# Kernel tuning notes

Hardware: AMD Instinct MI355X
Metric: run time of the kernel (lower is better)

Reference implementation:

```python
import jax, jax.numpy as jnp
import numpy as np

D, HALF, HID, COND, NBLK = 784, 392, 512, 10, 20
CLAMP = 1.0
B = 4096


def _linear_params(key, fan_in, fan_out, n):
    kw, kb = jax.random.split(key)
    lim = 1.0 / np.sqrt(fan_in)
    W = jax.random.uniform(kw, (n, fan_in, fan_out), minval=-lim, maxval=lim, dtype=jnp.float32)
    b = jax.random.uniform(kb, (n, fan_out), minval=-lim, maxval=lim, dtype=jnp.float32)
    return W, b


def setup_inputs() -> dict:
    key = jax.random.key(0)
    ks = jax.random.split(key, 6)
    x = jax.random.normal(ks[0], (B, 1, 28, 28), dtype=jnp.float32)
    l = jax.random.randint(ks[1], (B,), 0, 10)
    # FrEIA PermuteRandom: fixed permutation from numpy seed k per block
    perms = jnp.asarray(np.stack([np.random.RandomState(k).permutation(D) for k in range(NBLK)]), dtype=jnp.int32)
    s1_W1, s1_b1 = _linear_params(ks[2], HALF + COND, HID, NBLK)
    s1_W2, s1_b2 = _linear_params(ks[3], HID, 2 * HALF, NBLK)
    s2_W1, s2_b1 = _linear_params(ks[4], HALF + COND, HID, NBLK)
    s2_W2, s2_b2 = _linear_params(ks[5], HID, 2 * HALF, NBLK)
    return dict(x=x, l=l, perms=perms,
                s1_W1=s1_W1, s1_b1=s1_b1, s1_W2=s1_W2, s1_b2=s1_b2,
                s2_W1=s2_W1, s2_b1=s2_b1, s2_W2=s2_W2, s2_b2=s2_b2)


def _log_e(s):
    # FrEIA GLOW clamping: clamp * 0.636 * atan(s / clamp)
    return CLAMP * 0.636 * jnp.arctan(s / CLAMP)


def reference(x, l, perms, s1_W1, s1_b1, s1_W2, s1_b2, s2_W1, s2_b1, s2_W2, s2_b2):
    v = x.reshape(x.shape[0], D)  # Flatten
    c = jax.nn.one_hot(l, COND, dtype=v.dtype)  # one_hot condition [B,10]
    jac0 = jnp.zeros(v.shape[0], dtype=v.dtype)

    def block(carry, p):
        v, jac = carry
        perm, W1a, b1a, W1b, b1b, W2a, b2a, W2b, b2b = p
        v = v[:, perm]  # PermuteRandom (log-det 0)
        x1, x2 = v[:, :HALF], v[:, HALF:]
        # GLOWCouplingBlock forward
        r2 = jax.nn.relu(jnp.concatenate([x2, c], 1) @ W2a + b2a) @ W2b + b2b
        s2, t2 = r2[:, :HALF], r2[:, HALF:]
        ls2 = _log_e(s2)
        y1 = jnp.exp(ls2) * x1 + t2
        r1 = jax.nn.relu(jnp.concatenate([y1, c], 1) @ W1a + b1a) @ W1b + b1b
        s1, t1 = r1[:, :HALF], r1[:, HALF:]
        ls1 = _log_e(s1)
        y2 = jnp.exp(ls1) * x2 + t1
        jac = jac + ls1.sum(1) + ls2.sum(1)
        return (jnp.concatenate([y1, y2], 1), jac), None

    (z, jac), _ = jax.lax.scan(
        block, (v, jac0),
        (perms, s1_W1, s1_b1, s1_W2, s1_b2, s2_W1, s2_b1, s2_W2, s2_b2))
    return z, jac
```

## Files before the change

### kernel.cpp

```cpp
#include <hip/hip_runtime.h>

#define BN 4096
#define DF 784
#define HALFF 392
#define HIDF 512
#define NBLK 20
#define KS1 448
#define KS2 512
#define BT 16
#define NW 8
#define THREADS 512

#define Y1o 28672
#define Y2o 35840
#define Ho  43008
#define SMH 51200

typedef _Float16 f16;
typedef _Float16 half4v __attribute__((ext_vector_type(4)));
typedef _Float16 half8v __attribute__((ext_vector_type(8)));
typedef float    fx4    __attribute__((ext_vector_type(4)));
typedef int      ix4    __attribute__((ext_vector_type(4)));

__device__ __forceinline__ int lad(int base, int b, int k, int pitch)
{
    return base + b * pitch + (k & ~63) + ((((k >> 3) & 7) ^ (b & 7)) << 3) + (k & 7);
}

__global__ void pack1_k(const float* __restrict__ W1, f16* __restrict__ dst)
{
    const int m = blockIdx.y;
    const int nt = blockIdx.x / 14, sl = blockIdx.x % 14;
    const int l = threadIdx.x;
    const int n = nt * 16 + (l & 15);
    const int kb = sl * 32 + (l >> 4) * 8;
    const float* src = W1 + (long)m * 402 * 512;
    half8v o;
    #pragma unroll
    for (int e = 0; e < 8; e++) {
        int k = kb + e;
        o[e] = (k < HALFF) ? (f16)src[(long)k * 512 + n] : (f16)0.f;
    }
    *(half8v*)&dst[(((long)(m * 32 + nt) * 14) + sl) * 512 + l * 8] = o;
}

__global__ void pack2_k(const float* __restrict__ W2, f16* __restrict__ dst)
{
    const int m = blockIdx.y;
    const int dt = blockIdx.x / 16, sl = blockIdx.x % 16;
    const int c = threadIdx.x >> 6, l = threadIdx.x & 63;
    int dr = dt * 16 + (l & 15);
    if (dr >= HALFF) dr = HALFF - 1;
    const int d = dr + c * HALFF;
    const int kb = sl * 32 + (l >> 4) * 8;
    const float* src = W2 + (long)m * 512 * 784;
    half8v o;
    #pragma unroll
    for (int e = 0; e < 8; e++)
        o[e] = (f16)src[(long)(kb + e) * 784 + d];
    *(half8v*)&dst[((((long)(m * 25 + dt) * 16) + sl) * 2 + c) * 512 + l * 8] = o;
}

__global__ void prep_c16_k(const float* __restrict__ W1, const float* __restrict__ b1,
                           f16* __restrict__ dst)
{
    const int m = blockIdx.x;
    for (int idx = threadIdx.x; idx < 10 * HIDF; idx += 256) {
        int cls = idx >> 9, n = idx & 511;
        dst[(long)m * 10 * HIDF + idx] =
            (f16)(W1[(long)m * 402 * 512 + (long)(HALFF + cls) * 512 + n] + b1[(long)m * HIDF + n]);
    }
}

__global__ void inv_k(const int* __restrict__ perms, int* __restrict__ invp)
{
    const int i = blockIdx.x;
    for (int d = threadIdx.x; d < DF; d += 256) {
        int src = perms[(long)i * DF + d];
        invp[(long)i * DF + src] = d;
    }
}

__device__ __forceinline__ void do_gemm1(f16* SM, const f16* __restrict__ Wpk,
                                         const f16* __restrict__ C16,
                                         int Ao, int clsr, int wid, int lane,
                                         int ln16, int koct)
{
    half8v afr[14];
    #pragma unroll
    for (int sl = 0; sl < 14; sl++)
        afr[sl] = *(const half8v*)&SM[lad(Ao, ln16, sl * 32 + koct * 8, KS1)];

    const f16* base = Wpk + (long)wid * 4 * 14 * 512 + lane * 8;
    half8v wf[2][14];
    #pragma unroll
    for (int sl = 0; sl < 14; sl++)
        wf[0][sl] = *(const half8v*)&base[sl * 512];

    #pragma unroll
    for (int j = 0; j < 4; j++) {
        if (j < 3) {
            const f16* bn = base + (j + 1) * 14 * 512;
            #pragma unroll
            for (int sl = 0; sl < 14; sl++)
                wf[(j + 1) & 1][sl] = *(const half8v*)&bn[sl * 512];
        }
        fx4 acc = {};
        #pragma unroll
        for (int sl = 0; sl < 14; sl++)
            acc = __builtin_amdgcn_mfma_f32_16x16x32_f16(wf[j & 1][sl], afr[sl], acc, 0, 0, 0);
        int nb = wid * 64 + j * 16 + koct * 4;
        half4v c = *(const half4v*)&C16[clsr * HIDF + nb];
        half4v o;
        #pragma unroll
        for (int r = 0; r < 4; r++)
            o[r] = (f16)fmaxf(acc[r] + (float)c[r], 0.f);
        *(half4v*)&SM[lad(Ho, ln16, nb, HIDF)] = o;
    }
}

__device__ __forceinline__ float couple_store(f16* SM, const float* __restrict__ b2,
        const int* __restrict__ invz, int B1o_, int B2o_, int doScat,
        int Xmo, int Yo, int dbase, int ln16, fx4 sac, fx4 tac)
{
    float jp = 0.f;
    if (dbase + 3 < HALFF) {
        fx4 bs = *(const fx4*)&b2[dbase];
        fx4 bt = *(const fx4*)&b2[dbase + HALFF];
        half4v xv = *(const half4v*)&SM[lad(Xmo, ln16, dbase, KS1)];
        half4v o;
        #pragma unroll
        for (int r = 0; r < 4; r++) {
            float s  = sac[r] + bs[r];
            float tt = tac[r] + bt[r];
            float ls = 0.636f * atanf(s);
            jp += ls;
            o[r] = (f16)(expf(ls) * (float)xv[r] + tt);
        }
        *(half4v*)&SM[lad(Yo, ln16, dbase, KS1)] = o;
        if (doScat) {
            ix4 iv = *(const ix4*)&invz[dbase];
            #pragma unroll
            for (int r = 0; r < 4; r++) {
                int dp = iv[r];
                int dbo = (dp < HALFF) ? B1o_ : B2o_;
                int dk  = (dp < HALFF) ? dp : dp - HALFF;
                SM[lad(dbo, ln16, dk, KS1)] = o[r];
            }
        }
    }
    return jp;
}

__device__ __forceinline__ float do_gemm2(f16* SM, const f16* __restrict__ Wpk,
        const float* __restrict__ b2, const int* __restrict__ invz,
        int B1o_, int B2o_, int doScat, int Xmo, int Yo,
        int wid, int lane, int ln16, int koct)
{
    float jp = 0.f;
    #pragma unroll
    for (int j = 0; j < 4; j++) {
        const int dp = (j < 3) ? (wid + j * 8) : 24;
        const bool act = (j < 3) || (wid == 0);
        if (act) {
            const f16* bp = Wpk + (long)dp * (16 * 2 * 512) + lane * 8;
            half8v ws[16], wt[16];
            #pragma unroll
            for (int sl = 0; sl < 16; sl++)
                ws[sl] = *(const half8v*)&bp[(sl * 2) * 512];
            #pragma unroll
            for (int sl = 0; sl < 16; sl++)
                wt[sl] = *(const half8v*)&bp[(sl * 2 + 1) * 512];
            fx4 sac = {}, tac = {};
            #pragma unroll
            for (int sl = 0; sl < 16; sl++) {
                half8v h = *(const half8v*)&SM[lad(Ho, ln16, sl * 32 + koct * 8, HIDF)];
                sac = __builtin_amdgcn_mfma_f32_16x16x32_f16(ws[sl], h, sac, 0, 0, 0);
                tac = __builtin_amdgcn_mfma_f32_16x16x32_f16(wt[sl], h, tac, 0, 0, 0);
            }
            jp += couple_store(SM, b2, invz, B1o_, B2o_, doScat, Xmo, Yo,
                               dp * 16 + koct * 4, ln16, sac, tac);
        }
    }
    return jp;
}

__global__ __launch_bounds__(THREADS, 2)
void mega_k(const float* __restrict__ x, const int* __restrict__ lvec,
            const int* __restrict__ invp,
            const f16* __restrict__ Wf1a, const f16* __restrict__ Wf1b,
            const f16* __restrict__ Wf2a, const f16* __restrict__ Wf2b,
            const f16* __restrict__ C16a, const f16* __restrict__ C16b,
            const float* __restrict__ b2a, const float* __restrict__ b2b,
            float* __restrict__ outp)
{
    __shared__ __align__(16) f16 SM[SMH];
    __shared__ float JR[NW][BT];
    const int tid  = threadIdx.x;
    const int wid  = tid >> 6, lane = tid & 63;
    const int ln16 = lane & 15, koct = lane >> 4;
    const int b0g  = blockIdx.x * BT;
    const int clsr = lvec[b0g + ln16];

    int A1 = 0, A2 = 7168, B1 = 14336, B2 = 21504;

    half8v hz = {};
    for (int idx = tid; idx < 3 * BT * 7; idx += THREADS) {
        int buf = idx / (BT * 7);
        int rem = idx - buf * (BT * 7);
        int b = rem / 7, g = rem - (rem / 7) * 7;
        int base = (buf == 0) ? A2 : (buf == 1) ? B2 : Y1o;
        *(half8v*)&SM[lad(base, b, HALFF + g * 8, KS1)] = hz;
    }
    for (int idx = tid; idx < BT * (DF / 4); idx += THREADS) {
        int b = idx / (DF / 4);
        int q = (idx - b * (DF / 4)) * 4;
        fx4 v = *(const fx4*)&x[(long)(b0g + b) * DF + q];
        ix4 iv = *(const ix4*)&invp[q];
        #pragma unroll
        for (int r = 0; r < 4; r++) {
            int dp = iv[r];
            if (dp < HALFF) SM[lad(A1, b, dp, KS1)] = (f16)v[r];
            else            SM[lad(A2, b, dp - HALFF, KS1)] = (f16)v[r];
        }
    }
    __syncthreads();

    float jacc = 0.f;
    #pragma unroll 1
    for (int i = 0; i < NBLK; i++) {
        const int* ivz = invp + (long)((i + 1 < NBLK) ? (i + 1) : 0) * DF;
        const int doScat = (i + 1 < NBLK);
        do_gemm1(SM, Wf1a + (long)i * 32 * 14 * 512, C16a + (long)i * 10 * HIDF,
                 A2, clsr, wid, lane, ln16, koct);
        __syncthreads();
        jacc += do_gemm2(SM, Wf2a + (long)i * 25 * 16 * 2 * 512, b2a + (long)i * DF,
                         ivz, B1, B2, doScat, A1, Y1o, wid, lane, ln16, koct);
        __syncthreads();
        do_gemm1(SM, Wf1b + (long)i * 32 * 14 * 512, C16b + (long)i * 10 * HIDF,
                 Y1o, clsr, wid, lane, ln16, koct);
        __syncthreads();
        jacc += do_gemm2(SM, Wf2b + (long)i * 25 * 16 * 2 * 512, b2b + (long)i * DF,
                         ivz + HALFF, B1, B2, doScat, A2, Y2o, wid, lane, ln16, koct);
        __syncthreads();
        int t1 = A1; A1 = B1; B1 = t1;
        int t2 = A2; A2 = B2; B2 = t2;
    }

    for (int idx = tid; idx < BT * (DF / 4); idx += THREADS) {
        int b = idx / (DF / 4);
        int q = (idx - b * (DF / 4)) * 4;
        int so = (q < HALFF) ? Y1o : Y2o;
        int kk = (q < HALFF) ? q : q - HALFF;
        half4v v = *(const half4v*)&SM[lad(so, b, kk, KS1)];
        fx4 o;
        #pragma unroll
        for (int r = 0; r < 4; r++) o[r] = (float)v[r];
        *(fx4*)&outp[(long)(b0g + b) * DF + q] = o;
    }
    float j1 = jacc + __shfl_xor(jacc, 16);
    j1 += __shfl_xor(j1, 32);
    if (koct == 0) JR[wid][ln16] = j1;
    __syncthreads();
    if (tid < BT) {
        float s = 0.f;
        #pragma unroll
        for (int w = 0; w < NW; w++) s += JR[w][tid];
        outp[(long)BN * DF + b0g + tid] = s;
    }
}

extern "C" void kernel_launch(void* const* d_in, const int* in_sizes, int n_in,
                              void* d_out, int out_size, void* d_ws, size_t ws_size,
                              hipStream_t stream)
{
    const float* x     = (const float*)d_in[0];
    const int*   l     = (const int*)d_in[1];
    const int*   perms = (const int*)d_in[2];
    const float* s1W1  = (const float*)d_in[3];
    const float* s1b1  = (const float*)d_in[4];
    const float* s1W2  = (const float*)d_in[5];
    const float* s1b2  = (const float*)d_in[6];
    const float* s2W1  = (const float*)d_in[7];
    const float* s2b1  = (const float*)d_in[8];
    const float* s2W2  = (const float*)d_in[9];
    const float* s2b2  = (const float*)d_in[10];
    float* out = (float*)d_out;

    const long W1E = 32L * 14 * 512;
    const long W2E = 25L * 16 * 2 * 512;
    f16* Wf1a = (f16*)d_ws;
    f16* Wf1b = Wf1a + W1E * NBLK;
    f16* Wf2a = Wf1b + W1E * NBLK;
    f16* Wf2b = Wf2a + W2E * NBLK;
    f16* C16a = Wf2b + W2E * NBLK;
    f16* C16b = C16a + (long)NBLK * 10 * HIDF;
    int* invp = (int*)(C16b + (long)NBLK * 10 * HIDF);

    pack1_k<<<dim3(32 * 14, NBLK), 64, 0, stream>>>(s2W1, Wf1a);
    pack1_k<<<dim3(32 * 14, NBLK), 64, 0, stream>>>(s1W1, Wf1b);
    pack2_k<<<dim3(25 * 16, NBLK), 128, 0, stream>>>(s2W2, Wf2a);
    pack2_k<<<dim3(25 * 16, NBLK), 128, 0, stream>>>(s1W2, Wf2b);
    prep_c16_k<<<NBLK, 256, 0, stream>>>(s2W1, s2b1, C16a);
    prep_c16_k<<<NBLK, 256, 0, stream>>>(s1W1, s1b1, C16b);
    inv_k<<<NBLK, 256, 0, stream>>>(perms, invp);

    mega_k<<<BN / BT, THREADS, 0, stream>>>(x, l, invp,
            Wf1a, Wf1b, Wf2a, Wf2b, C16a, C16b, s2b2, s1b2, out);
}
```

Measured before the change: 841.0 us.

## Double waves per block, trim K slices, and write coupling outputs in place

Raises the block to 1024 threads (16 waves) so each wave computes fewer GEMM tiles, with launch bounds asking for higher occupancy. Lowers register pressure by no longer keeping A fragments and double-buffered weights in registers. GEMM2 now loads the s and t weights one after the other. GEMM1 drops from 14 to 13 K slices, since 13×32=416 still covers the 402-wide input. The Y1/Y2 shared buffers are removed and coupling outputs are written back in place into the A buffers, shrinking LDS use. In exchange, A fragments are re-read from LDS inside the MFMA loop, and the 16-way split of 25 output tiles leaves waves unevenly loaded.

```diff
diff --git a/kernel.cpp b/kernel.cpp
--- a/kernel.cpp
+++ b/kernel.cpp
@@ -5,16 +5,19 @@
 #define HALFF 392
 #define HIDF 512
 #define NBLK 20
-#define KS1 448
-#define KS2 512
+#define NSL1 13
+#define NSL2 16
+#define XP  448
 #define BT 16
-#define NW 8
-#define THREADS 512
-
-#define Y1o 28672
-#define Y2o 35840
-#define Ho  43008
-#define SMH 51200
+#define NW 16
+#define THREADS 1024
+
+#define A1o 0
+#define A2o 7168
+#define B1o 14336
+#define B2o 21504
+#define Ho  28672
+#define SMH 36864
 
 typedef _Float16 f16;
 typedef _Float16 half4v __attribute__((ext_vector_type(4)));
@@ -30,7 +33,7 @@
 __global__ void pack1_k(const float* __restrict__ W1, f16* __restrict__ dst)
 {
     const int m = blockIdx.y;
-    const int nt = blockIdx.x / 14, sl = blockIdx.x % 14;
+    const int nt = blockIdx.x / NSL1, sl = blockIdx.x % NSL1;
     const int l = threadIdx.x;
     const int n = nt * 16 + (l & 15);
     const int kb = sl * 32 + (l >> 4) * 8;
@@ -41,7 +44,7 @@
         int k = kb + e;
         o[e] = (k < HALFF) ? (f16)src[(long)k * 512 + n] : (f16)0.f;
     }
-    *(half8v*)&dst[(((long)(m * 32 + nt) * 14) + sl) * 512 + l * 8] = o;
+    *(half8v*)&dst[(((long)(m * 32 + nt) * NSL1) + sl) * 512 + l * 8] = o;
 }
 
 __global__ void pack2_k(const float* __restrict__ W2, f16* __restrict__ dst)
@@ -86,30 +89,21 @@
                                          int Ao, int clsr, int wid, int lane,
                                          int ln16, int koct)
 {
-    half8v afr[14];
     #pragma unroll
-    for (int sl = 0; sl < 14; sl++)
-        afr[sl] = *(const half8v*)&SM[lad(Ao, ln16, sl * 32 + koct * 8, KS1)];
-
-    const f16* base = Wpk + (long)wid * 4 * 14 * 512 + lane * 8;
-    half8v wf[2][14];
-    #pragma unroll
-    for (int sl = 0; sl < 14; sl++)
-        wf[0][sl] = *(const half8v*)&base[sl * 512];
-
-    #pragma unroll
-    for (int j = 0; j < 4; j++) {
-        if (j < 3) {
-            const f16* bn = base + (j + 1) * 14 * 512;
-            #pragma unroll
-            for (int sl = 0; sl < 14; sl++)
-                wf[(j + 1) & 1][sl] = *(const half8v*)&bn[sl * 512];
-        }
+    for (int j = 0; j < 2; j++) {
+        const int tile = wid * 2 + j;
+        const f16* bp = Wpk + ((long)tile * NSL1) * 512 + lane * 8;
+        half8v wf[NSL1];
+        #pragma unroll
+        for (int sl = 0; sl < NSL1; sl++)
+            wf[sl] = *(const half8v*)&bp[sl * 512];
         fx4 acc = {};
         #pragma unroll
-        for (int sl = 0; sl < 14; sl++)
-            acc = __builtin_amdgcn_mfma_f32_16x16x32_f16(wf[j & 1][sl], afr[sl], acc, 0, 0, 0);
-        int nb = wid * 64 + j * 16 + koct * 4;
+        for (int sl = 0; sl < NSL1; sl++) {
+            half8v a = *(const half8v*)&SM[lad(Ao, ln16, sl * 32 + koct * 8, XP)];
+            acc = __builtin_amdgcn_mfma_f32_16x16x32_f16(wf[sl], a, acc, 0, 0, 0);
+        }
+        const int nb = tile * 16 + koct * 4;
         half4v c = *(const half4v*)&C16[clsr * HIDF + nb];
         half4v o;
         #pragma unroll
@@ -120,14 +114,15 @@
 }
 
 __device__ __forceinline__ float couple_store(f16* SM, const float* __restrict__ b2,
-        const int* __restrict__ invz, int B1o_, int B2o_, int doScat,
-        int Xmo, int Yo, int dbase, int ln16, fx4 sac, fx4 tac)
+        const int* __restrict__ ivz, int B1_, int B2_, int doScat,
+        int Xmo, int dbase, int ln16, fx4 sac, fx4 tac)
 {
     float jp = 0.f;
     if (dbase + 3 < HALFF) {
         fx4 bs = *(const fx4*)&b2[dbase];
         fx4 bt = *(const fx4*)&b2[dbase + HALFF];
-        half4v xv = *(const half4v*)&SM[lad(Xmo, ln16, dbase, KS1)];
+        const int xa = lad(Xmo, ln16, dbase, XP);
+        half4v xv = *(const half4v*)&SM[xa];
         half4v o;
         #pragma unroll
         for (int r = 0; r < 4; r++) {
@@ -137,15 +132,15 @@
             jp += ls;
             o[r] = (f16)(expf(ls) * (float)xv[r] + tt);
         }
-        *(half4v*)&SM[lad(Yo, ln16, dbase, KS1)] = o;
+        *(half4v*)&SM[xa] = o;
         if (doScat) {
-            ix4 iv = *(const ix4*)&invz[dbase];
+            ix4 iv = *(const ix4*)&ivz[dbase];
             #pragma unroll
             for (int r = 0; r < 4; r++) {
                 int dp = iv[r];
-                int dbo = (dp < HALFF) ? B1o_ : B2o_;
+                int dbo = (dp < HALFF) ? B1_ : B2_;
                 int dk  = (dp < HALFF) ? dp : dp - HALFF;
-                SM[lad(dbo, ln16, dk, KS1)] = o[r];
+                SM[lad(dbo, ln16, dk, XP)] = o[r];
             }
         }
     }
@@ -153,39 +148,47 @@
 }
 
 __device__ __forceinline__ float do_gemm2(f16* SM, const f16* __restrict__ Wpk,
-        const float* __restrict__ b2, const int* __restrict__ invz,
-        int B1o_, int B2o_, int doScat, int Xmo, int Yo,
+        const float* __restrict__ b2, const int* __restrict__ ivz,
+        int B1_, int B2_, int doScat, int Xmo,
         int wid, int lane, int ln16, int koct)
 {
     float jp = 0.f;
     #pragma unroll
-    for (int j = 0; j < 4; j++) {
-        const int dp = (j < 3) ? (wid + j * 8) : 24;
-        const bool act = (j < 3) || (wid == 0);
-        if (act) {
-            const f16* bp = Wpk + (long)dp * (16 * 2 * 512) + lane * 8;
-            half8v ws[16], wt[16];
-            #pragma unroll
-            for (int sl = 0; sl < 16; sl++)
-                ws[sl] = *(const half8v*)&bp[(sl * 2) * 512];
-            #pragma unroll
-            for (int sl = 0; sl < 16; sl++)
-                wt[sl] = *(const half8v*)&bp[(sl * 2 + 1) * 512];
+    for (int rnd = 0; rnd < 2; rnd++) {
+        const int dp = wid + rnd * 16;
+        if (dp < 25) {
+            const f16* bp = Wpk + (long)dp * (NSL2 * 2 * 512) + lane * 8;
             fx4 sac = {}, tac = {};
-            #pragma unroll
-            for (int sl = 0; sl < 16; sl++) {
-                half8v h = *(const half8v*)&SM[lad(Ho, ln16, sl * 32 + koct * 8, HIDF)];
-                sac = __builtin_amdgcn_mfma_f32_16x16x32_f16(ws[sl], h, sac, 0, 0, 0);
-                tac = __builtin_amdgcn_mfma_f32_16x16x32_f16(wt[sl], h, tac, 0, 0, 0);
+            {
+                half8v w[NSL2];
+                #pragma unroll
+                for (int sl = 0; sl < NSL2; sl++)
+                    w[sl] = *(const half8v*)&bp[(sl * 2) * 512];
+                #pragma unroll
+                for (int sl = 0; sl < NSL2; sl++) {
+                    half8v h = *(const half8v*)&SM[lad(Ho, ln16, sl * 32 + koct * 8, HIDF)];
+                    sac = __builtin_amdgcn_mfma_f32_16x16x32_f16(w[sl], h, sac, 0, 0, 0);
+                }
             }
-            jp += couple_store(SM, b2, invz, B1o_, B2o_, doScat, Xmo, Yo,
+            {
+                half8v w[NSL2];
+                #pragma unroll
+                for (int sl = 0; sl < NSL2; sl++)
+                    w[sl] = *(const half8v*)&bp[(sl * 2 + 1) * 512];
+                #pragma unroll
+                for (int sl = 0; sl < NSL2; sl++) {
+                    half8v h = *(const half8v*)&SM[lad(Ho, ln16, sl * 32 + koct * 8, HIDF)];
+                    tac = __builtin_amdgcn_mfma_f32_16x16x32_f16(w[sl], h, tac, 0, 0, 0);
+                }
+            }
+            jp += couple_store(SM, b2, ivz, B1_, B2_, doScat, Xmo,
                                dp * 16 + koct * 4, ln16, sac, tac);
         }
     }
     return jp;
 }
 
-__global__ __launch_bounds__(THREADS, 2)
+__global__ __launch_bounds__(THREADS, 4)
 void mega_k(const float* __restrict__ x, const int* __restrict__ lvec,
             const int* __restrict__ invp,
             const f16* __restrict__ Wf1a, const f16* __restrict__ Wf1b,
@@ -202,15 +205,14 @@
     const int b0g  = blockIdx.x * BT;
     const int clsr = lvec[b0g + ln16];
 
-    int A1 = 0, A2 = 7168, B1 = 14336, B2 = 21504;
+    int A1 = A1o, A2 = A2o, B1 = B1o, B2 = B2o;
 
     half8v hz = {};
-    for (int idx = tid; idx < 3 * BT * 7; idx += THREADS) {
+    for (int idx = tid; idx < 4 * BT * 7; idx += THREADS) {
         int buf = idx / (BT * 7);
         int rem = idx - buf * (BT * 7);
         int b = rem / 7, g = rem - (rem / 7) * 7;
-        int base = (buf == 0) ? A2 : (buf == 1) ? B2 : Y1o;
-        *(half8v*)&SM[lad(base, b, HALFF + g * 8, KS1)] = hz;
+        *(half8v*)&SM[lad(buf * 7168, b, HALFF + g * 8, XP)] = hz;
     }
     for (int idx = tid; idx < BT * (DF / 4); idx += THREADS) {
         int b = idx / (DF / 4);
@@ -220,8 +222,8 @@
         #pragma unroll
         for (int r = 0; r < 4; r++) {
             int dp = iv[r];
-            if (dp < HALFF) SM[lad(A1, b, dp, KS1)] = (f16)v[r];
-            else            SM[lad(A2, b, dp - HALFF, KS1)] = (f16)v[r];
+            if (dp < HALFF) SM[lad(A1, b, dp, XP)] = (f16)v[r];
+            else            SM[lad(A2, b, dp - HALFF, XP)] = (f16)v[r];
         }
     }
     __syncthreads();
@@ -231,28 +233,30 @@
     for (int i = 0; i < NBLK; i++) {
         const int* ivz = invp + (long)((i + 1 < NBLK) ? (i + 1) : 0) * DF;
         const int doScat = (i + 1 < NBLK);
-        do_gemm1(SM, Wf1a + (long)i * 32 * 14 * 512, C16a + (long)i * 10 * HIDF,
+        do_gemm1(SM, Wf1a + (long)i * 32 * NSL1 * 512, C16a + (long)i * 10 * HIDF,
                  A2, clsr, wid, lane, ln16, koct);
         __syncthreads();
-        jacc += do_gemm2(SM, Wf2a + (long)i * 25 * 16 * 2 * 512, b2a + (long)i * DF,
-                         ivz, B1, B2, doScat, A1, Y1o, wid, lane, ln16, koct);
+        jacc += do_gemm2(SM, Wf2a + (long)i * 25 * NSL2 * 2 * 512, b2a + (long)i * DF,
+                         ivz, B1, B2, doScat, A1, wid, lane, ln16, koct);
         __syncthreads();
-        do_gemm1(SM, Wf1b + (long)i * 32 * 14 * 512, C16b + (long)i * 10 * HIDF,
-                 Y1o, clsr, wid, lane, ln16, koct);
+        do_gemm1(SM, Wf1b + (long)i * 32 * NSL1 * 512, C16b + (long)i * 10 * HIDF,
+                 A1, clsr, wid, lane, ln16, koct);
         __syncthreads();
-        jacc += do_gemm2(SM, Wf2b + (long)i * 25 * 16 * 2 * 512, b2b + (long)i * DF,
-                         ivz + HALFF, B1, B2, doScat, A2, Y2o, wid, lane, ln16, koct);
+        jacc += do_gemm2(SM, Wf2b + (long)i * 25 * NSL2 * 2 * 512, b2b + (long)i * DF,
+                         ivz + HALFF, B1, B2, doScat, A2, wid, lane, ln16, koct);
         __syncthreads();
-        int t1 = A1; A1 = B1; B1 = t1;
-        int t2 = A2; A2 = B2; B2 = t2;
+        if (i + 1 < NBLK) {
+            int t1 = A1; A1 = B1; B1 = t1;
+            int t2 = A2; A2 = B2; B2 = t2;
+        }
     }
 
     for (int idx = tid; idx < BT * (DF / 4); idx += THREADS) {
         int b = idx / (DF / 4);
         int q = (idx - b * (DF / 4)) * 4;
-        int so = (q < HALFF) ? Y1o : Y2o;
+        int so = (q < HALFF) ? A1 : A2;
         int kk = (q < HALFF) ? q : q - HALFF;
-        half4v v = *(const half4v*)&SM[lad(so, b, kk, KS1)];
+        half4v v = *(const half4v*)&SM[lad(so, b, kk, XP)];
         fx4 o;
         #pragma unroll
         for (int r = 0; r < 4; r++) o[r] = (float)v[r];
@@ -287,8 +291,8 @@
     const float* s2b2  = (const float*)d_in[10];
     float* out = (float*)d_out;
 
-    const long W1E = 32L * 14 * 512;
-    const long W2E = 25L * 16 * 2 * 512;
+    const long W1E = 32L * NSL1 * 512;
+    const long W2E = 25L * NSL2 * 2 * 512;
     f16* Wf1a = (f16*)d_ws;
     f16* Wf1b = Wf1a + W1E * NBLK;
     f16* Wf2a = Wf1b + W1E * NBLK;
@@ -297,8 +301,8 @@
     f16* C16b = C16a + (long)NBLK * 10 * HIDF;
     int* invp = (int*)(C16b + (long)NBLK * 10 * HIDF);
 
-    pack1_k<<<dim3(32 * 14, NBLK), 64, 0, stream>>>(s2W1, Wf1a);
-    pack1_k<<<dim3(32 * 14, NBLK), 64, 0, stream>>>(s1W1, Wf1b);
+    pack1_k<<<dim3(32 * NSL1, NBLK), 64, 0, stream>>>(s2W1, Wf1a);
+    pack1_k<<<dim3(32 * NSL1, NBLK), 64, 0, stream>>>(s1W1, Wf1b);
     pack2_k<<<dim3(25 * 16, NBLK), 128, 0, stream>>>(s2W2, Wf2a);
     pack2_k<<<dim3(25 * 16, NBLK), 128, 0, stream>>>(s1W2, Wf2b);
     prep_c16_k<<<NBLK, 256, 0, stream>>>(s2W1, s2b1, C16a);
```

After: 761.3 us. 1.1x faster.
